# Kernel tuning notes

Measured on AMD Instinct MI355X. Metric: run time of the kernel, lower is better.

## Reference

```python
import jax, jax.numpy as jnp
import numpy as np

NUM_COLORS = 10
COLOR_MAPPING_W = 0.4
CONSISTENCY_W = 0.3
RULE_W = 0.2
EXACT_BONUS = 5.0


def _color_rules(targets, num_colors):
    # Vectorized equivalent of per-batch torch.unique(): sorted unique colors
    # of each grid written into the first slots of a [B, 10] rules tensor.
    B = targets.shape[0]
    colors = jnp.arange(num_colors)
    presence = jnp.any(targets[:, :, :, None] == colors, axis=(1, 2))  # [B, 10]
    pos = jnp.cumsum(presence.astype(jnp.int32), axis=1) - 1           # slot index per color
    cols = jnp.where(presence, pos, num_colors)                        # absent -> dump slot
    rules = jnp.zeros((B, num_colors + 1), dtype=jnp.float32)
    rules = rules.at[jnp.arange(B)[:, None], cols].set(
        colors.astype(jnp.float32) * presence.astype(jnp.float32))
    return rules[:, :num_colors]


def setup_inputs() -> dict:
    key = jax.random.key(0)
    k1, k2, k3, k4 = jax.random.split(key, 4)
    B, C, H, W = 4096, NUM_COLORS, 30, 30
    return {
        "color_output": jax.random.normal(k1, (B, C, H, W), dtype=jnp.float32),
        "targets": jax.random.randint(k2, (B, H, W), 0, C),
        "color_attention": jax.random.uniform(k3, (B, H, W, C), dtype=jnp.float32),
        "lstm_rules": jax.random.normal(k4, (B, C), dtype=jnp.float32),
    }


def reference(color_output, targets, color_attention, lstm_rules):
    B, C, H, W = color_output.shape
    # exact-match cross entropy (mean over B*H*W)
    logp = jax.nn.log_softmax(color_output, axis=1)               # [B,C,H,W]
    ce = -jnp.take_along_axis(logp, targets[:, None], axis=1).mean()
    pred_colors = jnp.argmax(color_output, axis=1)                # [B,H,W]
    eq = (pred_colors == targets).astype(jnp.float32)
    exact_count = eq.sum()
    # color mapping: MSE(attention, one_hot(targets))
    onehot = jax.nn.one_hot(targets, C, dtype=jnp.float32)        # [B,H,W,C]
    color_mapping = jnp.mean((color_attention - onehot) ** 2)
    # sliding 2x2 window consistency, fused: avg over windows of (1 - mean eq)
    s = eq[:, :-1, :-1] + eq[:, 1:, :-1] + eq[:, :-1, 1:] + eq[:, 1:, 1:]
    consistency = 1.0 - s.mean() / 4.0
    # rule learning: MSE against per-batch sorted-unique-color rules
    rule_target = _color_rules(targets, C)
    rule_loss = jnp.mean((lstm_rules - rule_target) ** 2)
    total = (ce + COLOR_MAPPING_W * color_mapping
             + CONSISTENCY_W * consistency + RULE_W * rule_loss)
    total = total - (exact_count / B) * EXACT_BONUS  # bonus is 0 when count is 0
    total = jnp.maximum(total, 0.001)
    return (total, ce, color_mapping, consistency, rule_loss, exact_count)
```

## Files before the change

### kernel.cpp

```cpp
#include <hip/hip_runtime.h>


namespace {
constexpr int kB = 4096;
constexpr int kC = 10;
constexpr int kH = 30;
constexpr int kW = 30;
constexpr int kHW = kH * kW;
constexpr int kCHW = kC * kHW;
constexpr int kQuadsPerB = kHW / 4;
constexpr int kQuads = kB * kQuadsPerB;
constexpr int kThreads = 256;
constexpr int kGrid = 1800;
constexpr int kQPT = 2;
static_assert(kGrid * kThreads * kQPT == kQuads, "work split must be exact");
}

__global__ __launch_bounds__(kThreads) void iris_fused(
    const float* __restrict__ logits_g,
    const int* __restrict__ targets_g,
    const float* __restrict__ att_g,
    float* __restrict__ ce_part,
    float* __restrict__ cmat_part,
    float* __restrict__ cmsq_part,
    unsigned* __restrict__ weq_part,
    unsigned* __restrict__ eq_part)
{
    const int tid = threadIdx.x;
    const int gid = blockIdx.x * kThreads + tid;

    float ce_acc = 0.f, at_acc = 0.f, sq_acc = 0.f;
    unsigned weq_acc = 0u, eq_acc = 0u;

#pragma unroll
    for (int k = 0; k < kQPT; ++k) {
        const int q = gid + k * (kGrid * kThreads);
        const int b = q / kQuadsPerB;
        const int i = q - b * kQuadsPerB;
        const int p0 = 4 * i;

        const int4 tv = *reinterpret_cast<const int4*>(targets_g + (size_t)b * kHW + p0);
        const int ta[4] = {tv.x, tv.y, tv.z, tv.w};

        const float* __restrict__ ap = att_g + (size_t)b * kCHW + (size_t)p0 * kC;
        float atq[4] = {0.f, 0.f, 0.f, 0.f};
#pragma unroll
        for (int u = 0; u < kC; ++u) {
            const float4 v = *reinterpret_cast<const float4*>(ap + 4 * u);
            const float av[4] = {v.x, v.y, v.z, v.w};
#pragma unroll
            for (int e2 = 0; e2 < 4; ++e2) {
                const int e = 4 * u + e2;
                const int j = e / kC;
                const int ch = e - j * kC;
                sq_acc += av[e2] * av[e2];
                atq[j] = (ch == ta[j]) ? av[e2] : atq[j];
            }
        }
        at_acc += atq[0] + atq[1] + atq[2] + atq[3];

        const float* __restrict__ lg = logits_g + (size_t)b * kCHW + p0;
        float m[4], s[4], xt[4];
        int am[4];
#pragma unroll
        for (int j = 0; j < 4; ++j) { m[j] = -3.4e38f; s[j] = 0.f; xt[j] = 0.f; am[j] = 0; }
#pragma unroll
        for (int c = 0; c < kC; ++c) {
            const float4 v = *reinterpret_cast<const float4*>(lg + c * kHW);
            const float xv[4] = {v.x, v.y, v.z, v.w};
#pragma unroll
            for (int j = 0; j < 4; ++j) {
                const bool gt = xv[j] > m[j];
                const float mn = gt ? xv[j] : m[j];
                s[j] = s[j] * __expf(m[j] - mn) + __expf(xv[j] - mn);
                m[j] = mn;
                am[j] = gt ? c : am[j];
                xt[j] = (c == ta[j]) ? xv[j] : xt[j];
            }
        }
#pragma unroll
        for (int j = 0; j < 4; ++j) {
            ce_acc += m[j] + __logf(s[j]) - xt[j];
            const unsigned eq = (am[j] == ta[j]) ? 1u : 0u;
            eq_acc += eq;
            const int p = p0 + j;
            const int h = p / kW;
            const int w = p - h * kW;
            weq_acc += eq * (((h == 0 || h == kH - 1) ? 1u : 2u) *
                             ((w == 0 || w == kW - 1) ? 1u : 2u));
        }
    }

#pragma unroll
    for (int off = 32; off > 0; off >>= 1) {
        ce_acc  += __shfl_down(ce_acc, off);
        at_acc  += __shfl_down(at_acc, off);
        sq_acc  += __shfl_down(sq_acc, off);
        weq_acc += __shfl_down(weq_acc, off);
        eq_acc  += __shfl_down(eq_acc, off);
    }
    __shared__ float sf[3][4];
    __shared__ unsigned su[2][4];
    const int wave = tid >> 6;
    if ((tid & 63) == 0) {
        sf[0][wave] = ce_acc; sf[1][wave] = at_acc; sf[2][wave] = sq_acc;
        su[0][wave] = weq_acc; su[1][wave] = eq_acc;
    }
    __syncthreads();
    if (tid == 0) {
        ce_part[blockIdx.x]   = sf[0][0] + sf[0][1] + sf[0][2] + sf[0][3];
        cmat_part[blockIdx.x] = sf[1][0] + sf[1][1] + sf[1][2] + sf[1][3];
        cmsq_part[blockIdx.x] = sf[2][0] + sf[2][1] + sf[2][2] + sf[2][3];
        weq_part[blockIdx.x]  = su[0][0] + su[0][1] + su[0][2] + su[0][3];
        eq_part[blockIdx.x]   = su[1][0] + su[1][1] + su[1][2] + su[1][3];
    }
}

__global__ __launch_bounds__(64) void iris_rules(
    const int* __restrict__ targets_g, const float* __restrict__ rules_g,
    float* __restrict__ rule_part) {
    const int b = blockIdx.x;
    const int lane = threadIdx.x;
    const int* __restrict__ tgt = targets_g + (size_t)b * kHW;
    unsigned mask = 0u;
    for (int k = lane; k < kHW; k += 64) mask |= 1u << tgt[k];
#pragma unroll
    for (int off = 32; off > 0; off >>= 1) mask |= __shfl_down(mask, off);
    if (lane == 0) {
        const float* __restrict__ lr = rules_g + (size_t)b * kC;
        unsigned mrem = mask;
        float rl = 0.f;
#pragma unroll
        for (int s2 = 0; s2 < kC; ++s2) {
            float v = 0.f;
            if (mrem) {
                v = (float)(__ffs(mrem) - 1);
                mrem &= mrem - 1u;
            }
            const float d = lr[s2] - v;
            rl += d * d;
        }
        rule_part[b] = rl;
    }
}

__global__ __launch_bounds__(1024) void iris_finalize(
    const float* __restrict__ ce_part,
    const float* __restrict__ cmat_part,
    const float* __restrict__ cmsq_part,
    const unsigned* __restrict__ weq_part,
    const unsigned* __restrict__ eq_part,
    const float* __restrict__ rule_part,
    float* __restrict__ out) {
    const int tid = threadIdx.x;
    double ce = 0.0, cma = 0.0, cms = 0.0, rl = 0.0;
    unsigned long long weq = 0ull, eqc = 0ull;
    for (int i = tid; i < kGrid; i += 1024) {
        ce  += (double)ce_part[i];
        cma += (double)cmat_part[i];
        cms += (double)cmsq_part[i];
        weq += (unsigned long long)weq_part[i];
        eqc += (unsigned long long)eq_part[i];
    }
#pragma unroll
    for (int k = 0; k < 4; ++k) rl += (double)rule_part[tid + 1024 * k];
#pragma unroll
    for (int off = 32; off > 0; off >>= 1) {
        ce  += __shfl_down(ce, off);
        cma += __shfl_down(cma, off);
        cms += __shfl_down(cms, off);
        rl  += __shfl_down(rl, off);
        weq += __shfl_down(weq, off);
        eqc += __shfl_down(eqc, off);
    }
    __shared__ double sd[4][16];
    __shared__ unsigned long long su[2][16];
    const int wave = tid >> 6;
    if ((tid & 63) == 0) {
        sd[0][wave] = ce; sd[1][wave] = cma; sd[2][wave] = cms; sd[3][wave] = rl;
        su[0][wave] = weq; su[1][wave] = eqc;
    }
    __syncthreads();
    if (tid == 0) {
        ce = 0.0; cma = 0.0; cms = 0.0; rl = 0.0; weq = 0ull; eqc = 0ull;
#pragma unroll
        for (int i = 0; i < 16; ++i) {
            ce += sd[0][i]; cma += sd[1][i]; cms += sd[2][i]; rl += sd[3][i];
            weq += su[0][i]; eqc += su[1][i];
        }
        const double npix = (double)kB * kHW;
        const double ce_m = ce / npix;
        const double cm_m = (cms - 2.0 * cma + npix) / (npix * kC);
        const double s_mean = (double)weq / ((double)kB * (kH - 1) * (kW - 1));
        const double cons = 1.0 - s_mean / 4.0;
        const double rl_m = rl / ((double)kB * kC);
        const double exact = (double)eqc;
        double total = ce_m + 0.4 * cm_m + 0.3 * cons + 0.2 * rl_m
                       - (exact / (double)kB) * 5.0;
        if (total < 0.001) total = 0.001;
        out[0] = (float)total;
        out[1] = (float)ce_m;
        out[2] = (float)cm_m;
        out[3] = (float)cons;
        out[4] = (float)rl_m;
        out[5] = (float)exact;
    }
}

extern "C" void kernel_launch(void* const* d_in, const int* in_sizes, int n_in,
                              void* d_out, int out_size, void* d_ws, size_t ws_size,
                              hipStream_t stream) {
    const float* color_output    = (const float*)d_in[0];
    const int*   targets         = (const int*)d_in[1];
    const float* color_attention = (const float*)d_in[2];
    const float* lstm_rules      = (const float*)d_in[3];
    float* out = (float*)d_out;

    float*    ce_part   = (float*)d_ws;
    float*    cmat_part = ce_part + kGrid;
    float*    cmsq_part = cmat_part + kGrid;
    unsigned* weq_part  = (unsigned*)(cmsq_part + kGrid);
    unsigned* eq_part   = weq_part + kGrid;
    float*    rule_part = (float*)(eq_part + kGrid);

    iris_fused<<<kGrid, kThreads, 0, stream>>>(color_output, targets, color_attention,
                                               ce_part, cmat_part, cmsq_part,
                                               weq_part, eq_part);
    iris_rules<<<kB, 64, 0, stream>>>(targets, lstm_rules, rule_part);
    iris_finalize<<<1, 1024, 0, stream>>>(ce_part, cmat_part, cmsq_part,
                                          weq_part, eq_part, rule_part, out);
}
```

Baseline: 341.6 us.

## Stage attention through LDS with coalesced loads and one pixel per thread

Each block now loads its contiguous attention slice with fully coalesced float4 loads into shared memory, accumulates the squared sum there, and then gathers the target-channel value from LDS. The previous per-thread strided 160-byte reads are gone. Logits are processed one pixel per lane with scalar coalesced loads, and the online softmax becomes a two-pass max-then-sum. This adds 20KB of LDS per block and extra barriers, which may limit occupancy, and it replaces 128-bit logit loads with 32-bit ones.

```diff
diff --git a/kernel.cpp b/kernel.cpp
--- a/kernel.cpp
+++ b/kernel.cpp
@@ -8,13 +8,16 @@
 constexpr int kW = 30;
 constexpr int kHW = kH * kW;
 constexpr int kCHW = kC * kHW;
-constexpr int kQuadsPerB = kHW / 4;
-constexpr int kQuads = kB * kQuadsPerB;
+constexpr int kPix = kB * kHW;
 constexpr int kThreads = 256;
-constexpr int kGrid = 1800;
-constexpr int kQPT = 2;
-static_assert(kGrid * kThreads * kQPT == kQuads, "work split must be exact");
-}
+constexpr int kPPT = 2;
+constexpr int kPixPerBlk = kThreads * kPPT;
+constexpr int kGridF = kPix / kPixPerBlk;
+static_assert(kGridF * kPixPerBlk == kPix, "exact split");
+constexpr int kAttFlt = kPixPerBlk * kC;
+}
+
+typedef float f32x4 __attribute__((ext_vector_type(4)));
 
 __global__ __launch_bounds__(kThreads) void iris_fused(
     const float* __restrict__ logits_g,
@@ -26,69 +29,65 @@
     unsigned* __restrict__ weq_part,
     unsigned* __restrict__ eq_part)
 {
+    __shared__ float lds_att[kAttFlt];
     const int tid = threadIdx.x;
-    const int gid = blockIdx.x * kThreads + tid;
-
-    float ce_acc = 0.f, at_acc = 0.f, sq_acc = 0.f;
+    const int blk = blockIdx.x;
+
+    const float* __restrict__ ab = att_g + (size_t)blk * kAttFlt;
+    float sq_acc = 0.f;
+#pragma unroll
+    for (int k = 0; k < 5; ++k) {
+        const int f4 = tid + kThreads * k;
+        const f32x4 v = *reinterpret_cast<const f32x4*>(ab + 4 * f4);
+        sq_acc += v[0] * v[0] + v[1] * v[1] + v[2] * v[2] + v[3] * v[3];
+        *reinterpret_cast<f32x4*>(lds_att + 4 * f4) = v;
+    }
+
+    float ce_acc = 0.f;
     unsigned weq_acc = 0u, eq_acc = 0u;
-
-#pragma unroll
-    for (int k = 0; k < kQPT; ++k) {
-        const int q = gid + k * (kGrid * kThreads);
-        const int b = q / kQuadsPerB;
-        const int i = q - b * kQuadsPerB;
-        const int p0 = 4 * i;
-
-        const int4 tv = *reinterpret_cast<const int4*>(targets_g + (size_t)b * kHW + p0);
-        const int ta[4] = {tv.x, tv.y, tv.z, tv.w};
-
-        const float* __restrict__ ap = att_g + (size_t)b * kCHW + (size_t)p0 * kC;
-        float atq[4] = {0.f, 0.f, 0.f, 0.f};
-#pragma unroll
-        for (int u = 0; u < kC; ++u) {
-            const float4 v = *reinterpret_cast<const float4*>(ap + 4 * u);
-            const float av[4] = {v.x, v.y, v.z, v.w};
-#pragma unroll
-            for (int e2 = 0; e2 < 4; ++e2) {
-                const int e = 4 * u + e2;
-                const int j = e / kC;
-                const int ch = e - j * kC;
-                sq_acc += av[e2] * av[e2];
-                atq[j] = (ch == ta[j]) ? av[e2] : atq[j];
-            }
+    int tsv[kPPT];
+#pragma unroll
+    for (int u = 0; u < kPPT; ++u) {
+        const int p = blk * kPixPerBlk + tid + kThreads * u;
+        const int b = p / kHW;
+        const int i = p - b * kHW;
+        const int t = targets_g[p];
+        tsv[u] = t;
+
+        const float* __restrict__ lg = logits_g + (size_t)b * kCHW + i;
+        float x[kC];
+#pragma unroll
+        for (int c = 0; c < kC; ++c) x[c] = lg[c * kHW];
+
+        float m = x[0];
+        int am = 0;
+        float xt = (t == 0) ? x[0] : 0.f;
+#pragma unroll
+        for (int c = 1; c < kC; ++c) {
+            const bool gt = x[c] > m;
+            am = gt ? c : am;
+            m = gt ? x[c] : m;
+            xt = (c == t) ? x[c] : xt;
         }
-        at_acc += atq[0] + atq[1] + atq[2] + atq[3];
-
-        const float* __restrict__ lg = logits_g + (size_t)b * kCHW + p0;
-        float m[4], s[4], xt[4];
-        int am[4];
-#pragma unroll
-        for (int j = 0; j < 4; ++j) { m[j] = -3.4e38f; s[j] = 0.f; xt[j] = 0.f; am[j] = 0; }
-#pragma unroll
-        for (int c = 0; c < kC; ++c) {
-            const float4 v = *reinterpret_cast<const float4*>(lg + c * kHW);
-            const float xv[4] = {v.x, v.y, v.z, v.w};
-#pragma unroll
-            for (int j = 0; j < 4; ++j) {
-                const bool gt = xv[j] > m[j];
-                const float mn = gt ? xv[j] : m[j];
-                s[j] = s[j] * __expf(m[j] - mn) + __expf(xv[j] - mn);
-                m[j] = mn;
-                am[j] = gt ? c : am[j];
-                xt[j] = (c == ta[j]) ? xv[j] : xt[j];
-            }
-        }
-#pragma unroll
-        for (int j = 0; j < 4; ++j) {
-            ce_acc += m[j] + __logf(s[j]) - xt[j];
-            const unsigned eq = (am[j] == ta[j]) ? 1u : 0u;
-            eq_acc += eq;
-            const int p = p0 + j;
-            const int h = p / kW;
-            const int w = p - h * kW;
-            weq_acc += eq * (((h == 0 || h == kH - 1) ? 1u : 2u) *
-                             ((w == 0 || w == kW - 1) ? 1u : 2u));
-        }
+        float s = 0.f;
+#pragma unroll
+        for (int c = 0; c < kC; ++c) s += __expf(x[c] - m);
+        ce_acc += m + __logf(s) - xt;
+
+        const unsigned eq = (am == t) ? 1u : 0u;
+        eq_acc += eq;
+        const int h = i / kW;
+        const int w = i - h * kW;
+        weq_acc += eq * (((h == 0 || h == kH - 1) ? 1u : 2u) *
+                         ((w == 0 || w == kW - 1) ? 1u : 2u));
+    }
+
+    __syncthreads();
+    float at_acc = 0.f;
+#pragma unroll
+    for (int u = 0; u < kPPT; ++u) {
+        const int p_local = tid + kThreads * u;
+        at_acc += lds_att[p_local * kC + tsv[u]];
     }
 
 #pragma unroll
@@ -99,20 +98,24 @@
         weq_acc += __shfl_down(weq_acc, off);
         eq_acc  += __shfl_down(eq_acc, off);
     }
-    __shared__ float sf[3][4];
-    __shared__ unsigned su[2][4];
+    __syncthreads();
+    float* rf = lds_att;
+    unsigned* ru = reinterpret_cast<unsigned*>(lds_att + 12);
     const int wave = tid >> 6;
     if ((tid & 63) == 0) {
-        sf[0][wave] = ce_acc; sf[1][wave] = at_acc; sf[2][wave] = sq_acc;
-        su[0][wave] = weq_acc; su[1][wave] = eq_acc;
+        rf[wave] = ce_acc;
+        rf[4 + wave] = at_acc;
+        rf[8 + wave] = sq_acc;
+        ru[wave] = weq_acc;
+        ru[4 + wave] = eq_acc;
     }
     __syncthreads();
     if (tid == 0) {
-        ce_part[blockIdx.x]   = sf[0][0] + sf[0][1] + sf[0][2] + sf[0][3];
-        cmat_part[blockIdx.x] = sf[1][0] + sf[1][1] + sf[1][2] + sf[1][3];
-        cmsq_part[blockIdx.x] = sf[2][0] + sf[2][1] + sf[2][2] + sf[2][3];
-        weq_part[blockIdx.x]  = su[0][0] + su[0][1] + su[0][2] + su[0][3];
-        eq_part[blockIdx.x]   = su[1][0] + su[1][1] + su[1][2] + su[1][3];
+        ce_part[blk]   = rf[0] + rf[1] + rf[2] + rf[3];
+        cmat_part[blk] = rf[4] + rf[5] + rf[6] + rf[7];
+        cmsq_part[blk] = rf[8] + rf[9] + rf[10] + rf[11];
+        weq_part[blk]  = ru[0] + ru[1] + ru[2] + ru[3];
+        eq_part[blk]   = ru[4] + ru[5] + ru[6] + ru[7];
     }
 }
 
@@ -155,7 +158,7 @@
     const int tid = threadIdx.x;
     double ce = 0.0, cma = 0.0, cms = 0.0, rl = 0.0;
     unsigned long long weq = 0ull, eqc = 0ull;
-    for (int i = tid; i < kGrid; i += 1024) {
+    for (int i = tid; i < kGridF; i += 1024) {
         ce  += (double)ce_part[i];
         cma += (double)cmat_part[i];
         cms += (double)cmsq_part[i];
@@ -217,15 +220,16 @@
     float* out = (float*)d_out;
 
     float*    ce_part   = (float*)d_ws;
-    float*    cmat_part = ce_part + kGrid;
-    float*    cmsq_part = cmat_part + kGrid;
-    unsigned* weq_part  = (unsigned*)(cmsq_part + kGrid);
-    unsigned* eq_part   = weq_part + kGrid;
-    float*    rule_part = (float*)(eq_part + kGrid);
-
-    iris_fused<<<kGrid, kThreads, 0, stream>>>(color_output, targets, color_attention,
-                                               ce_part, cmat_part, cmsq_part,
-                                               weq_part, eq_part);
+    float*    cmat_part = ce_part + kGridF;
+    float*    cmsq_part = cmat_part + kGridF;
+    unsigned* weq_part  = (unsigned*)(cmsq_part + kGridF);
+    unsigned* eq_part   = weq_part + kGridF;
+    float*    rule_part = (float*)(eq_part + kGridF);
+
+    iris_fused<<<kGridF, kThreads, 0, stream>>>(color_output, targets,
+                                                color_attention, ce_part,
+                                                cmat_part, cmsq_part,
+                                                weq_part, eq_part);
     iris_rules<<<kB, 64, 0, stream>>>(targets, lstm_rules, rule_part);
     iris_finalize<<<1, 1024, 0, stream>>>(ce_part, cmat_part, cmsq_part,
                                           weq_part, eq_part, rule_part, out);
```

Result: faster. 330.7 us (-3.2%).

## Issue all loads upfront, one quad per thread, two-pass softmax

Applied to the files above, without the earlier changes.

Each thread now handles a single quad, so the grid doubles to 3600 blocks. All 21 vector loads for that quad are issued at the start, and an empty asm barrier keeps the compiler from interleaving them with compute. The online-softmax rescaling is replaced by a max/argmax pass followed by an exp-sum pass, which removes the extra exp per channel. The cost is higher register pressure, bounded by a launch-bounds occupancy hint. A side effect is that the finalize kernel now reduces 3600 partials instead of 1800.

```diff
diff --git a/kernel.cpp b/kernel.cpp
--- a/kernel.cpp
+++ b/kernel.cpp
@@ -11,12 +11,14 @@
 constexpr int kQuadsPerB = kHW / 4;
 constexpr int kQuads = kB * kQuadsPerB;
 constexpr int kThreads = 256;
-constexpr int kGrid = 1800;
-constexpr int kQPT = 2;
-static_assert(kGrid * kThreads * kQPT == kQuads, "work split must be exact");
-}
-
-__global__ __launch_bounds__(kThreads) void iris_fused(
+constexpr int kGrid = kQuads / kThreads;
+static_assert(kGrid * kThreads == kQuads, "exact split");
+}
+
+typedef float f32x4 __attribute__((ext_vector_type(4)));
+typedef int i32x4 __attribute__((ext_vector_type(4)));
+
+__global__ __launch_bounds__(kThreads, 4) void iris_fused(
     const float* __restrict__ logits_g,
     const int* __restrict__ targets_g,
     const float* __restrict__ att_g,
@@ -27,68 +29,98 @@
     unsigned* __restrict__ eq_part)
 {
     const int tid = threadIdx.x;
-    const int gid = blockIdx.x * kThreads + tid;
-
-    float ce_acc = 0.f, at_acc = 0.f, sq_acc = 0.f;
+    const int q = blockIdx.x * kThreads + tid;
+    const int b = q / kQuadsPerB;
+    const int i = q - b * kQuadsPerB;
+    const int p0 = 4 * i;
+
+    const float* __restrict__ ap = att_g + (size_t)b * kCHW + (size_t)p0 * kC;
+    const float* __restrict__ lg = logits_g + (size_t)b * kCHW + p0;
+
+    i32x4 tv = *reinterpret_cast<const i32x4*>(targets_g + (size_t)b * kHW + p0);
+    f32x4 a0 = *reinterpret_cast<const f32x4*>(ap + 0);
+    f32x4 a1 = *reinterpret_cast<const f32x4*>(ap + 4);
+    f32x4 a2 = *reinterpret_cast<const f32x4*>(ap + 8);
+    f32x4 a3 = *reinterpret_cast<const f32x4*>(ap + 12);
+    f32x4 a4 = *reinterpret_cast<const f32x4*>(ap + 16);
+    f32x4 a5 = *reinterpret_cast<const f32x4*>(ap + 20);
+    f32x4 a6 = *reinterpret_cast<const f32x4*>(ap + 24);
+    f32x4 a7 = *reinterpret_cast<const f32x4*>(ap + 28);
+    f32x4 a8 = *reinterpret_cast<const f32x4*>(ap + 32);
+    f32x4 a9 = *reinterpret_cast<const f32x4*>(ap + 36);
+    f32x4 x0 = *reinterpret_cast<const f32x4*>(lg + 0 * kHW);
+    f32x4 x1 = *reinterpret_cast<const f32x4*>(lg + 1 * kHW);
+    f32x4 x2 = *reinterpret_cast<const f32x4*>(lg + 2 * kHW);
+    f32x4 x3 = *reinterpret_cast<const f32x4*>(lg + 3 * kHW);
+    f32x4 x4 = *reinterpret_cast<const f32x4*>(lg + 4 * kHW);
+    f32x4 x5 = *reinterpret_cast<const f32x4*>(lg + 5 * kHW);
+    f32x4 x6 = *reinterpret_cast<const f32x4*>(lg + 6 * kHW);
+    f32x4 x7 = *reinterpret_cast<const f32x4*>(lg + 7 * kHW);
+    f32x4 x8 = *reinterpret_cast<const f32x4*>(lg + 8 * kHW);
+    f32x4 x9 = *reinterpret_cast<const f32x4*>(lg + 9 * kHW);
+
+    asm volatile("" : "+v"(tv),
+                      "+v"(a0), "+v"(a1), "+v"(a2), "+v"(a3), "+v"(a4),
+                      "+v"(a5), "+v"(a6), "+v"(a7), "+v"(a8), "+v"(a9),
+                      "+v"(x0), "+v"(x1), "+v"(x2), "+v"(x3), "+v"(x4),
+                      "+v"(x5), "+v"(x6), "+v"(x7), "+v"(x8), "+v"(x9));
+
+    const int ta[4] = {tv[0], tv[1], tv[2], tv[3]};
+
+    float sq_acc = 0.f;
+    float atq[4] = {0.f, 0.f, 0.f, 0.f};
+#define IRIS_ATT(u, au)                                                        \
+    _Pragma("unroll")                                                          \
+    for (int e2 = 0; e2 < 4; ++e2) {                                           \
+        const int e = 4 * (u) + e2;                                            \
+        const int jx = e / kC;                                                 \
+        const int ch = e - jx * kC;                                            \
+        sq_acc += au[e2] * au[e2];                                             \
+        atq[jx] = (ch == ta[jx]) ? au[e2] : atq[jx];                           \
+    }
+    IRIS_ATT(0, a0) IRIS_ATT(1, a1) IRIS_ATT(2, a2) IRIS_ATT(3, a3)
+    IRIS_ATT(4, a4) IRIS_ATT(5, a5) IRIS_ATT(6, a6) IRIS_ATT(7, a7)
+    IRIS_ATT(8, a8) IRIS_ATT(9, a9)
+#undef IRIS_ATT
+    float at_acc = atq[0] + atq[1] + atq[2] + atq[3];
+
+    float m[4] = {x0[0], x0[1], x0[2], x0[3]};
+    float xt[4];
+    int am[4] = {0, 0, 0, 0};
+#pragma unroll
+    for (int j = 0; j < 4; ++j) xt[j] = (ta[j] == 0) ? x0[j] : 0.f;
+#define IRIS_P1(c, xc)                                                         \
+    _Pragma("unroll")                                                          \
+    for (int j = 0; j < 4; ++j) {                                              \
+        const bool gt = xc[j] > m[j];           \
+        am[j] = gt ? (c) : am[j];                                              \
+        m[j] = gt ? xc[j] : m[j];                                              \
+        xt[j] = ((c) == ta[j]) ? xc[j] : xt[j];                                \
+    }
+    IRIS_P1(1, x1) IRIS_P1(2, x2) IRIS_P1(3, x3) IRIS_P1(4, x4)
+    IRIS_P1(5, x5) IRIS_P1(6, x6) IRIS_P1(7, x7) IRIS_P1(8, x8)
+    IRIS_P1(9, x9)
+#undef IRIS_P1
+    float s[4] = {0.f, 0.f, 0.f, 0.f};
+#define IRIS_P2(xc)                                                            \
+    _Pragma("unroll")                                                          \
+    for (int j = 0; j < 4; ++j) s[j] += __expf(xc[j] - m[j]);
+    IRIS_P2(x0) IRIS_P2(x1) IRIS_P2(x2) IRIS_P2(x3) IRIS_P2(x4)
+    IRIS_P2(x5) IRIS_P2(x6) IRIS_P2(x7) IRIS_P2(x8) IRIS_P2(x9)
+#undef IRIS_P2
+
+    float ce_acc = 0.f;
     unsigned weq_acc = 0u, eq_acc = 0u;
-
-#pragma unroll
-    for (int k = 0; k < kQPT; ++k) {
-        const int q = gid + k * (kGrid * kThreads);
-        const int b = q / kQuadsPerB;
-        const int i = q - b * kQuadsPerB;
-        const int p0 = 4 * i;
-
-        const int4 tv = *reinterpret_cast<const int4*>(targets_g + (size_t)b * kHW + p0);
-        const int ta[4] = {tv.x, tv.y, tv.z, tv.w};
-
-        const float* __restrict__ ap = att_g + (size_t)b * kCHW + (size_t)p0 * kC;
-        float atq[4] = {0.f, 0.f, 0.f, 0.f};
-#pragma unroll
-        for (int u = 0; u < kC; ++u) {
-            const float4 v = *reinterpret_cast<const float4*>(ap + 4 * u);
-            const float av[4] = {v.x, v.y, v.z, v.w};
-#pragma unroll
-            for (int e2 = 0; e2 < 4; ++e2) {
-                const int e = 4 * u + e2;
-                const int j = e / kC;
-                const int ch = e - j * kC;
-                sq_acc += av[e2] * av[e2];
-                atq[j] = (ch == ta[j]) ? av[e2] : atq[j];
-            }
-        }
-        at_acc += atq[0] + atq[1] + atq[2] + atq[3];
-
-        const float* __restrict__ lg = logits_g + (size_t)b * kCHW + p0;
-        float m[4], s[4], xt[4];
-        int am[4];
-#pragma unroll
-        for (int j = 0; j < 4; ++j) { m[j] = -3.4e38f; s[j] = 0.f; xt[j] = 0.f; am[j] = 0; }
-#pragma unroll
-        for (int c = 0; c < kC; ++c) {
-            const float4 v = *reinterpret_cast<const float4*>(lg + c * kHW);
-            const float xv[4] = {v.x, v.y, v.z, v.w};
-#pragma unroll
-            for (int j = 0; j < 4; ++j) {
-                const bool gt = xv[j] > m[j];
-                const float mn = gt ? xv[j] : m[j];
-                s[j] = s[j] * __expf(m[j] - mn) + __expf(xv[j] - mn);
-                m[j] = mn;
-                am[j] = gt ? c : am[j];
-                xt[j] = (c == ta[j]) ? xv[j] : xt[j];
-            }
-        }
-#pragma unroll
-        for (int j = 0; j < 4; ++j) {
-            ce_acc += m[j] + __logf(s[j]) - xt[j];
-            const unsigned eq = (am[j] == ta[j]) ? 1u : 0u;
-            eq_acc += eq;
-            const int p = p0 + j;
-            const int h = p / kW;
-            const int w = p - h * kW;
-            weq_acc += eq * (((h == 0 || h == kH - 1) ? 1u : 2u) *
-                             ((w == 0 || w == kW - 1) ? 1u : 2u));
-        }
+#pragma unroll
+    for (int j = 0; j < 4; ++j) {
+        ce_acc += m[j] + __logf(s[j]) - xt[j];
+        const unsigned eq = (am[j] == ta[j]) ? 1u : 0u;
+        eq_acc += eq;
+        const int p = p0 + j;
+        const int h = p / kW;
+        const int w = p - h * kW;
+        weq_acc += eq * (((h == 0 || h == kH - 1) ? 1u : 2u) *
+                         ((w == 0 || w == kW - 1) ? 1u : 2u));
     }
 
 #pragma unroll
@@ -223,8 +255,9 @@
     unsigned* eq_part   = weq_part + kGrid;
     float*    rule_part = (float*)(eq_part + kGrid);
 
-    iris_fused<<<kGrid, kThreads, 0, stream>>>(color_output, targets, color_attention,
-                                               ce_part, cmat_part, cmsq_part,
+    iris_fused<<<kGrid, kThreads, 0, stream>>>(color_output, targets,
+                                               color_attention, ce_part,
+                                               cmat_part, cmsq_part,
                                                weq_part, eq_part);
     iris_rules<<<kB, 64, 0, stream>>>(targets, lstm_rules, rule_part);
     iris_finalize<<<1, 1024, 0, stream>>>(ce_part, cmat_part, cmsq_part,
```

Result: faster. 328.4 us (-3.9%).
